# Kernel tuning notes

Measured on AMD Instinct MI355X. Metric: run time of the kernel, lower is better.

The kernel has to match this reference:

```python
import jax, jax.numpy as jnp
import numpy as np

HEADS = 8
DIM_HEAD = 40


def setup_inputs() -> dict:
    key = jax.random.key(0)
    ks = jax.random.split(key, 10)
    b, n, j, qd, cd = 8, 4096, 77, 320, 768
    inner = HEADS * DIM_HEAD  # 320
    x = jax.random.normal(ks[0], (b, n, qd), jnp.float32)
    embs = jax.random.normal(ks[1], (b, j, cd), jnp.float32)
    Wq = jax.random.normal(ks[2], (qd, inner), jnp.float32) * 0.02
    Wk = jax.random.normal(ks[3], (cd, inner), jnp.float32) * 0.02
    Wv = jax.random.normal(ks[4], (cd, inner), jnp.float32) * 0.02
    Wo = jax.random.normal(ks[5], (inner, qd), jnp.float32) * 0.02
    bo = jnp.zeros((qd,), jnp.float32)
    # per-query-token, per-key-token additive attention mask (float weights)
    cross_attn_mask = (jax.random.uniform(ks[6], (b, n, j)) < 0.5).astype(jnp.float32)
    strength = jnp.ones((1,), jnp.float32) * 0.8
    # captiontypes >= 0 marks valid key tokens; include some -1 (invalid)
    captiontypes = jax.random.randint(ks[7], (b, j), -1, 3).at[:, 0].set(0)
    global_prompt_mask = (jax.random.uniform(ks[8], (b, j)) > 0.05).at[:, 0].set(True)
    return {"x": x, "embs": embs, "Wq": Wq, "Wk": Wk, "Wv": Wv, "Wo": Wo,
            "bo": bo, "cross_attn_mask": cross_attn_mask, "strength": strength,
            "captiontypes": captiontypes, "global_prompt_mask": global_prompt_mask}


def _split_heads(t):
    # [b, n, h*d] -> [(b h), n, d], head index fastest (matches einops '(b h)')
    b, n, _ = t.shape
    return t.reshape(b, n, HEADS, DIM_HEAD).transpose(0, 2, 1, 3).reshape(b * HEADS, n, DIM_HEAD)


def reference(x, embs, Wq, Wk, Wv, Wo, bo, cross_attn_mask, strength,
              captiontypes, global_prompt_mask):
    b, n, _ = x.shape
    scale = DIM_HEAD ** -0.5
    q = _split_heads(x @ Wq).astype(jnp.float32)   # [(b h), n, d]
    k = _split_heads(embs @ Wk).astype(jnp.float32)  # [(b h), j, d]
    v = _split_heads(embs @ Wv)                      # [(b h), j, d]
    sim = jnp.einsum('bid,bjd->bij', q, k)           # [(b h), n, j] fp32

    NEG = -jnp.finfo(sim.dtype).max
    key_mask = captiontypes >= 0                     # [b, j]
    key_mask_bh = jnp.repeat(key_mask, HEADS, axis=0)[:, None, :]  # [(b h), 1, j]

    # masked std of sim over valid key positions (unbiased, ddof=1), no grad
    w = jnp.broadcast_to(key_mask_bh, sim.shape).astype(sim.dtype)
    cnt = jnp.sum(w)
    mean = jnp.sum(sim * w) / cnt
    var = jnp.sum(w * (sim - mean) ** 2) / (cnt - 1.0)
    simstd = jnp.sqrt(var)

    wf = cross_attn_mask * simstd * strength[0]      # [b, n, j]
    wf = jnp.where(global_prompt_mask[:, None, :], wf, NEG)
    wf = jnp.repeat(wf, HEADS, axis=0)               # [(b h), n, j]
    wf = jax.lax.stop_gradient(wf)

    sim = jnp.where(key_mask_bh, sim, NEG) + wf
    attn = jax.nn.softmax(sim * scale, axis=-1)
    out = jnp.einsum('bij,bjd->bid', attn, v)        # [(b h), n, d]
    out = out.reshape(b, HEADS, n, DIM_HEAD).transpose(0, 2, 1, 3).reshape(b, n, HEADS * DIM_HEAD)
    return out @ Wo + bo
```

## Files before the change

### kernel.cpp

```cpp
#include <hip/hip_runtime.h>
#include <hip/hip_bf16.h>
#include <math.h>

#define HEADS 8
#define DIMH 40
#define BB 8
#define NN 4096
#define JJ 77
#define CDIM 768
#define INNER 320
#define NEGF (-3.4028234663852886e38f)

using bf16 = __hip_bfloat16;
using f32x4 = __attribute__((ext_vector_type(4))) float;
using bf16x8 = __attribute__((ext_vector_type(8))) short;
using ushort8 = __attribute__((ext_vector_type(8))) unsigned short;
using ushort4v = __attribute__((ext_vector_type(4))) unsigned short;

__device__ __forceinline__ unsigned short f2u(float f){
    bf16 t = __float2bfloat16(f);
    return *reinterpret_cast<unsigned short*>(&t);
}
__device__ __forceinline__ float u2f(unsigned short u){
    unsigned int w = ((unsigned int)u) << 16;
    return __uint_as_float(w);
}

struct Stats { int validcnt; int gflag; float simstd; };

__global__ void prep_kernel(const int* ct, const int* gpm, Stats* st){
    __shared__ int sflag, scnt;
    if(threadIdx.x==0){ sflag=0; scnt=0; }
    __syncthreads();
    int lflag=0, lcnt=0;
    for(int i=threadIdx.x;i<154;i+=blockDim.x){
        int g = gpm[i];
        if(g!=0 && g!=1) lflag=1;
    }
    for(int i=threadIdx.x;i<BB*JJ;i+=blockDim.x){
        if(ct[i]>=0) lcnt++;
    }
    if(lflag) atomicOr(&sflag,1);
    atomicAdd(&scnt,lcnt);
    __syncthreads();
    if(threadIdx.x==0){ st->validcnt=scnt; st->gflag=sflag; }
}

__global__ __launch_bounds__(256) void prep_weights(const float* __restrict__ Wq,
                                                    const float* __restrict__ Wo,
                                                    const float* __restrict__ Wk,
                                                    const float* __restrict__ Wv,
                                                    unsigned short* __restrict__ WqT,
                                                    unsigned short* __restrict__ WoT,
                                                    unsigned short* __restrict__ WkvT){
    __shared__ float tile[32][33];
    int blk = blockIdx.x;
    int tx = threadIdx.x & 31, ty = threadIdx.x >> 5;
    if(blk < 200){
        const float* in = (blk<100)? Wq : Wo;
        unsigned short* out = (blk<100)? WqT : WoT;
        int base = (blk<100)? blk : blk-100;
        int bx = base%10, by = base/10;
        int c0 = bx*32, r0 = by*32;
        #pragma unroll
        for(int i=0;i<32;i+=8) tile[ty+i][tx] = in[(size_t)(r0+ty+i)*320 + c0+tx];
        __syncthreads();
        #pragma unroll
        for(int i=0;i<32;i+=8) out[(size_t)(c0+ty+i)*320 + r0+tx] = f2u(tile[tx][ty+i]);
    } else {
        int local = blk-200;
        int nt = local%20, kt = local/20;
        int n0 = nt*32, k0 = kt*32;
        const float* in = (n0<320)? Wk : Wv;
        int nc0 = (n0<320)? n0 : n0-320;
        #pragma unroll
        for(int i=0;i<32;i+=8) tile[ty+i][tx] = in[(size_t)(k0+ty+i)*320 + nc0+tx];
        __syncthreads();
        #pragma unroll
        for(int i=0;i<32;i+=8) WkvT[(size_t)(n0+ty+i)*768 + k0+tx] = f2u(tile[tx][ty+i]);
    }
}

__global__ __launch_bounds__(256) void proj_kv_mfma(const float* __restrict__ embs,
                                                    const unsigned short* __restrict__ WkvT,
                                                    unsigned short* __restrict__ kws,
                                                    unsigned short* __restrict__ vt){
    __shared__ unsigned short As[64][40];
    __shared__ unsigned short Bs[64][40];
    int t = threadIdx.x;
    int bm = blockIdx.x % 10;
    int bn = blockIdx.x / 10;
    int row0 = bm*64, col0 = bn*64;
    int wave=t>>6, lane=t&63, l15=lane&15, lk=lane>>4;

    f32x4 acc[4];
    #pragma unroll
    for(int nf=0;nf<4;nf++) acc[nf]=(f32x4){0.f,0.f,0.f,0.f};

    for(int k0=0;k0<768;k0+=32){
        #pragma unroll
        for(int p=0;p<2;p++){
            int li = (p*256+t)*4; int r = li>>5, kk = li&31;
            int gr = row0 + r;
            ushort4v u;
            if(gr < 616){
                float4 v = *(const float4*)&embs[(size_t)gr*768 + k0+kk];
                u.x=f2u(v.x); u.y=f2u(v.y); u.z=f2u(v.z); u.w=f2u(v.w);
            } else { u.x=0;u.y=0;u.z=0;u.w=0; }
            *(ushort4v*)&As[r][kk] = u;
        }
        {
            int nn = t>>2, kk = (t&3)*8;
            *(ushort8*)&Bs[nn][kk] = *(const ushort8*)&WkvT[(size_t)(col0+nn)*768 + k0+kk];
        }
        __syncthreads();
        bf16x8 aF = *(const bf16x8*)&As[wave*16+l15][lk*8];
        #pragma unroll
        for(int nf=0;nf<4;nf++){
            bf16x8 bF = *(const bf16x8*)&Bs[nf*16+l15][lk*8];
            acc[nf] = __builtin_amdgcn_mfma_f32_16x16x32_bf16(aF,bF,acc[nf],0,0,0);
        }
        __syncthreads();
    }
    #pragma unroll
    for(int nf=0;nf<4;nf++){
        int col = col0 + nf*16 + l15;
        #pragma unroll
        for(int r=0;r<4;r++){
            int m = row0 + wave*16 + lk*4 + r;
            if(m < 616){
                int b = m/77, j = m - 77*b;
                unsigned short val = f2u(acc[nf][r]);
                if(col < 320){
                    int h = col/40, d = col - 40*h;
                    kws[(((size_t)b*HEADS+h)*JJ + j)*DIMH + d] = val;
                } else {
                    int c2 = col-320; int h = c2/40, d = c2 - 40*h;
                    size_t vbase = (((size_t)b*HEADS+h)*DIMH + d)*80;
                    vt[vbase + j] = val;
                    if(j==76){ vt[vbase+77]=0; vt[vbase+78]=0; vt[vbase+79]=0; }
                }
            }
        }
    }
}

template<int A_MODE, int C_MODE>
__global__ __launch_bounds__(256) void gemm_mfma(const void* __restrict__ A,
                                                 const unsigned short* __restrict__ Bt,
                                                 const float* __restrict__ bias,
                                                 void* __restrict__ C){
    __shared__ unsigned short As[128][40];
    __shared__ unsigned short Bs[64][40];
    int t = threadIdx.x;
    int bm = blockIdx.x & 255;
    int bn = blockIdx.x >> 8;
    int row0 = bm*128, col0 = bn*64;
    int wave = t>>6, lane = t&63;
    int wm = wave>>1, wn = wave&1;
    int l15 = lane&15, lk = lane>>4;

    f32x4 acc[4][2];
    #pragma unroll
    for(int i=0;i<4;i++)
        #pragma unroll
        for(int j=0;j<2;j++) acc[i][j] = (f32x4){0.f,0.f,0.f,0.f};

    for(int k0=0;k0<320;k0+=32){
        if(A_MODE==2){
            const unsigned short* Ab = (const unsigned short*)A;
            #pragma unroll
            for(int p=0;p<2;p++){
                int li = (p*256+t)*8; int r = li>>5, kk = li&31;
                int m = row0+r; int k = k0+kk;
                int b = m>>12, n = m&4095;
                int h = k/40, d = k-40*h;
                *(ushort8*)&As[r][kk] = *(const ushort8*)&Ab[(((size_t)(b*8+h))*NN + n)*DIMH + d];
            }
        } else {
            const float* Af = (const float*)A;
            #pragma unroll
            for(int p=0;p<4;p++){
                int li = (p*256+t)*4; int r = li>>5, kk = li&31;
                float4 v = *(const float4*)&Af[(size_t)(row0+r)*320 + k0+kk];
                ushort4v u; u.x=f2u(v.x); u.y=f2u(v.y); u.z=f2u(v.z); u.w=f2u(v.w);
                *(ushort4v*)&As[r][kk] = u;
            }
        }
        {
            int nn = t>>2, kk = (t&3)*8;
            *(ushort8*)&Bs[nn][kk] = *(const ushort8*)&Bt[(size_t)(col0+nn)*320 + k0+kk];
        }
        __syncthreads();
        bf16x8 a[4], b[2];
        #pragma unroll
        for(int mf=0;mf<4;mf++) a[mf] = *(const bf16x8*)&As[wm*64+mf*16+l15][lk*8];
        #pragma unroll
        for(int nf=0;nf<2;nf++) b[nf] = *(const bf16x8*)&Bs[wn*32+nf*16+l15][lk*8];
        #pragma unroll
        for(int mf=0;mf<4;mf++)
            #pragma unroll
            for(int nf=0;nf<2;nf++)
                acc[mf][nf] = __builtin_amdgcn_mfma_f32_16x16x32_bf16(a[mf], b[nf], acc[mf][nf], 0,0,0);
        __syncthreads();
    }
    if(C_MODE==1){
        float* Cf = (float*)C;
        float bv[2];
        #pragma unroll
        for(int nf=0;nf<2;nf++) bv[nf] = bias[col0+wn*32+nf*16+l15];
        #pragma unroll
        for(int mf=0;mf<4;mf++)
            #pragma unroll
            for(int nf=0;nf<2;nf++){
                int col = col0+wn*32+nf*16+l15;
                #pragma unroll
                for(int r=0;r<4;r++){
                    int m = row0+wm*64+mf*16+lk*4+r;
                    Cf[(size_t)m*320+col] = acc[mf][nf][r] + bv[nf];
                }
            }
    } else {
        unsigned short* Cb = (unsigned short*)C;
        #pragma unroll
        for(int mf=0;mf<4;mf++)
            #pragma unroll
            for(int nf=0;nf<2;nf++){
                int col = col0+wn*32+nf*16+l15;
                int h = col/40, d = col-40*h;
                #pragma unroll
                for(int r=0;r<4;r++){
                    int m = row0+wm*64+mf*16+lk*4+r;
                    int b = m>>12, n = m&4095;
                    Cb[(((size_t)(b*8+h))*NN + n)*DIMH + d] = f2u(acc[mf][nf][r]);
                }
            }
    }
}

__global__ __launch_bounds__(256) void stats_mfma(const unsigned short* __restrict__ qh,
                                                  const unsigned short* __restrict__ kws,
                                                  const int* __restrict__ ct,
                                                  float2* __restrict__ partials){
    int bh = blockIdx.x;
    int b = bh>>3;
    int t = threadIdx.x;
    int wave=t>>6, lane=t&63, l15=lane&15, lk=lane>>4;
    int wq0 = wave*16;
    bf16x8 zb = {0,0,0,0,0,0,0,0};

    int n0 = blockIdx.y*64;
    size_t qrow = ((size_t)bh*NN + n0 + wq0 + l15)*DIMH;
    bf16x8 aF0 = *(const bf16x8*)&qh[qrow + lk*8];
    bf16x8 aF1 = (lk==0) ? *(const bf16x8*)&qh[qrow + 32] : zb;

    bool kv[5];
    bf16x8 bK[2][5];
    #pragma unroll
    for(int jt=0;jt<5;jt++){
        int j = jt*16+l15;
        kv[jt] = (j<JJ) && (ct[b*JJ+j]>=0);
        #pragma unroll
        for(int ks=0;ks<2;ks++){
            if(j<JJ && !(ks==1 && lk>=1))
                bK[ks][jt] = *(const bf16x8*)&kws[((size_t)bh*JJ + j)*DIMH + ks*32 + lk*8];
            else bK[ks][jt] = zb;
        }
    }
    f32x4 sacc[5];
    #pragma unroll
    for(int jt=0;jt<5;jt++) sacc[jt]=(f32x4){0.f,0.f,0.f,0.f};
    #pragma unroll
    for(int jt=0;jt<5;jt++){
        sacc[jt] = __builtin_amdgcn_mfma_f32_16x16x32_bf16(aF0,bK[0][jt],sacc[jt],0,0,0);
        sacc[jt] = __builtin_amdgcn_mfma_f32_16x16x32_bf16(aF1,bK[1][jt],sacc[jt],0,0,0);
    }
    float s1=0.f, s2=0.f;
    #pragma unroll
    for(int jt=0;jt<5;jt++){
        if(kv[jt]){
            #pragma unroll
            for(int r=0;r<4;r++){ float v=sacc[jt][r]; s1+=v; s2+=v*v; }
        }
    }
    #pragma unroll
    for(int off=32;off>0;off>>=1){ s1 += __shfl_down(s1,off); s2 += __shfl_down(s2,off); }
    __shared__ float sa[4], sb[4];
    if(lane==0){ sa[wave]=s1; sb[wave]=s2; }
    __syncthreads();
    if(t==0){
        partials[blockIdx.y*64 + blockIdx.x] =
            make_float2(sa[0]+sa[1]+sa[2]+sa[3], sb[0]+sb[1]+sb[2]+sb[3]);
    }
}

__global__ __launch_bounds__(256) void finalize_kernel(const float2* __restrict__ partials,
                                                       const int* __restrict__ ct,
                                                       const int* __restrict__ gpm,
                                                       const float* __restrict__ strength,
                                                       Stats* st,
                                                       float* __restrict__ kmT,
                                                       float* __restrict__ adT,
                                                       float* __restrict__ gmT){
    int t = threadIdx.x;
    double s1=0.0, s2=0.0;
    for(int i=t;i<4096;i+=256){
        float2 p = partials[i];
        s1 += (double)p.x; s2 += (double)p.y;
    }
    #pragma unroll
    for(int off=32;off>0;off>>=1){ s1 += __shfl_down(s1,off); s2 += __shfl_down(s2,off); }
    __shared__ double da[4], db[4];
    __shared__ float s_simstd;
    int lane=t&63, w=t>>6;
    if(lane==0){ da[w]=s1; db[w]=s2; }
    __syncthreads();
    if(t==0){
        double S1 = da[0]+da[1]+da[2]+da[3];
        double S2 = db[0]+db[1]+db[2]+db[3];
        double cnt = (double)st->validcnt * HEADS * NN;
        double var = (S2 - S1*S1/cnt)/(cnt-1.0);
        float sd = (float)sqrt(var);
        st->simstd = sd;
        s_simstd = sd;
    }
    __syncthreads();
    float c = s_simstd * strength[0];
    int gflag = st->gflag;
    for(int i=t;i<BB*80;i+=256){
        int b = i/80, j = i-80*b;
        int kvv=0, gv=0;
        if(j<JJ){
            kvv = ct[b*JJ+j]>=0;
            gv = gflag ? (((const unsigned char*)gpm)[b*JJ+j]!=0) : (gpm[b*JJ+j]!=0);
        }
        kmT[i] = (j<JJ && kvv)?1.f:0.f;
        adT[i] = ((j<JJ && kvv)?0.f:NEGF) + ((j<JJ && gv)?0.f:NEGF);
        gmT[i] = (j<JJ && gv)? c : 0.f;
    }
}

__global__ __launch_bounds__(256) void attn_mfma(unsigned short* qh,
                                                 const unsigned short* __restrict__ kws,
                                                 const unsigned short* __restrict__ vt,
                                                 const float* __restrict__ cam,
                                                 const float* __restrict__ kmT,
                                                 const float* __restrict__ adT,
                                                 const float* __restrict__ gmT){
    int bh = blockIdx.x;
    int b = bh>>3;
    __shared__ unsigned short P[64][104];
    int t = threadIdx.x;
    int wave=t>>6, lane=t&63, l15=lane&15, lk=lane>>4;
    int wq0 = wave*16;
    bf16x8 zb = {0,0,0,0,0,0,0,0};
    ushort8 z8 = {0,0,0,0,0,0,0,0};

    int n0 = blockIdx.y*64;
    size_t qrow = ((size_t)bh*NN + n0 + wq0 + l15)*DIMH;
    bf16x8 aF0 = *(const bf16x8*)&qh[qrow + lk*8];
    bf16x8 aF1 = (lk==0) ? *(const bf16x8*)&qh[qrow + 32] : zb;

    float cv[5][4];
    #pragma unroll
    for(int jt=0;jt<5;jt++){
        int j = jt*16+l15; int jc = (j<JJ)? j : 76;
        #pragma unroll
        for(int r=0;r<4;r++){
            int row = n0 + wq0 + 4*lk + r;
            cv[jt][r] = cam[((size_t)b*NN+row)*JJ + jc];
        }
    }
    float km[5], gm[5], ad[5];
    #pragma unroll
    for(int jt=0;jt<5;jt++){
        int j = jt*16+l15;
        km[jt] = kmT[b*80+j]; ad[jt] = adT[b*80+j]; gm[jt] = gmT[b*80+j];
    }
    bf16x8 bK[2][5];
    #pragma unroll
    for(int ks=0;ks<2;ks++)
        #pragma unroll
        for(int jt=0;jt<5;jt++){
            int j = jt*16+l15;
            if(j<JJ && !(ks==1 && lk>=1))
                bK[ks][jt] = *(const bf16x8*)&kws[((size_t)bh*JJ + j)*DIMH + ks*32 + lk*8];
            else bK[ks][jt] = zb;
        }
    bf16x8 bV[3][3];
    #pragma unroll
    for(int ks=0;ks<3;ks++)
        #pragma unroll
        for(int nt=0;nt<3;nt++){
            int d = nt*16+l15;
            if(d<DIMH && !(ks==2 && lk>=2))
                bV[ks][nt] = *(const bf16x8*)&vt[((size_t)bh*DIMH + d)*80 + ks*32 + lk*8];
            else bV[ks][nt] = zb;
        }
    if(t<64){ *(ushort8*)&P[t][80]=z8; *(ushort8*)&P[t][88]=z8; *(ushort8*)&P[t][96]=z8; }

    const float scale = 0.15811388300841897f;
    f32x4 sacc[5];
    #pragma unroll
    for(int jt=0;jt<5;jt++) sacc[jt]=(f32x4){0.f,0.f,0.f,0.f};
    #pragma unroll
    for(int jt=0;jt<5;jt++){
        sacc[jt] = __builtin_amdgcn_mfma_f32_16x16x32_bf16(aF0,bK[0][jt],sacc[jt],0,0,0);
        sacc[jt] = __builtin_amdgcn_mfma_f32_16x16x32_bf16(aF1,bK[1][jt],sacc[jt],0,0,0);
    }
    float lo[5][4];
    #pragma unroll
    for(int jt=0;jt<5;jt++){
        #pragma unroll
        for(int r=0;r<4;r++)
            lo[jt][r] = (sacc[jt][r]*km[jt] + cv[jt][r]*gm[jt] + ad[jt])*scale;
    }
    float dinv[4];
    #pragma unroll
    for(int r=0;r<4;r++){
        float m = lo[0][r];
        #pragma unroll
        for(int jt=1;jt<5;jt++) m = fmaxf(m, lo[jt][r]);
        #pragma unroll
        for(int msk=1;msk<16;msk<<=1) m = fmaxf(m, __shfl_xor(m,msk));
        float s=0.f;
        #pragma unroll
        for(int jt=0;jt<5;jt++){ float e=__expf(lo[jt][r]-m); lo[jt][r]=e; s+=e; }
        #pragma unroll
        for(int msk=1;msk<16;msk<<=1) s += __shfl_xor(s,msk);
        dinv[r]=1.f/s;
    }
    #pragma unroll
    for(int jt=0;jt<5;jt++){
        int j = jt*16+l15;
        #pragma unroll
        for(int r=0;r<4;r++) P[wq0+4*lk+r][j] = f2u(lo[jt][r]*dinv[r]);
    }
    __syncthreads();
    f32x4 oacc[3];
    #pragma unroll
    for(int nt=0;nt<3;nt++) oacc[nt]=(f32x4){0.f,0.f,0.f,0.f};
    #pragma unroll
    for(int ks=0;ks<3;ks++){
        bf16x8 aP = *(const bf16x8*)&P[wq0+l15][ks*32+lk*8];
        #pragma unroll
        for(int nt=0;nt<3;nt++)
            oacc[nt] = __builtin_amdgcn_mfma_f32_16x16x32_bf16(aP,bV[ks][nt],oacc[nt],0,0,0);
    }
    #pragma unroll
    for(int nt=0;nt<3;nt++){
        int d = nt*16+l15;
        #pragma unroll
        for(int r=0;r<4;r++){
            unsigned short ush = f2u(oacc[nt][r]);
            int other = __shfl_xor((int)ush, 1);
            if((l15&1)==0 && d<DIMH){
                unsigned int word = (unsigned int)ush | (((unsigned int)(unsigned short)other)<<16);
                int row = n0 + wq0 + 4*lk + r;
                *(unsigned int*)&qh[((size_t)bh*NN + row)*DIMH + d] = word;
            }
        }
    }
}

extern "C" void kernel_launch(void* const* d_in, const int* in_sizes, int n_in,
                              void* d_out, int out_size, void* d_ws, size_t ws_size,
                              hipStream_t stream) {
    const float* x        = (const float*)d_in[0];
    const float* embs     = (const float*)d_in[1];
    const float* Wq       = (const float*)d_in[2];
    const float* Wk       = (const float*)d_in[3];
    const float* Wv       = (const float*)d_in[4];
    const float* Wo       = (const float*)d_in[5];
    const float* bo       = (const float*)d_in[6];
    const float* cam      = (const float*)d_in[7];
    const float* strength = (const float*)d_in[8];
    const int*  ct       = (const int*)d_in[9];
    const int*  gpm      = (const int*)d_in[10];

    char* ws = (char*)d_ws;
    unsigned short* qh   = (unsigned short*)ws;
    unsigned short* kws  = (unsigned short*)(ws + 20971520);
    unsigned short* vt   = (unsigned short*)(ws + 21365760);
    unsigned short* WqT  = (unsigned short*)(ws + 21775360);
    unsigned short* WoT  = (unsigned short*)(ws + 21980160);
    unsigned short* WkvT = (unsigned short*)(ws + 22184960);
    Stats* st  = (Stats*)(ws + 23168000);
    float2* partials = (float2*)(ws + 23169024);
    float* kmT = (float*)(ws + 23201792);
    float* adT = (float*)(ws + 23204352);
    float* gmT = (float*)(ws + 23206912);

    prep_kernel<<<1,256,0,stream>>>(ct,gpm,st);
    prep_weights<<<680,256,0,stream>>>(Wq,Wo,Wk,Wv,WqT,WoT,WkvT);
    proj_kv_mfma<<<100,256,0,stream>>>(embs,WkvT,kws,vt);
    gemm_mfma<0,2><<<1280,256,0,stream>>>(x,WqT,nullptr,qh);
    stats_mfma<<<dim3(64,64),256,0,stream>>>(qh,kws,ct,partials);
    finalize_kernel<<<1,256,0,stream>>>(partials,ct,gpm,strength,st,kmT,adT,gmT);
    attn_mfma<<<dim3(64,64),256,0,stream>>>(qh,kws,vt,cam,kmT,adT,gmT);
    gemm_mfma<2,1><<<1280,256,0,stream>>>(qh,WoT,bo,d_out);
}
```

Baseline: 130.2 us.

## Enlarge GEMM tile to 256x64 and fold prep kernel into finalize

The projection GEMMs now use 256-row tiles, with each wave computing a 64x64 output block, which halves the block count and reuses each B fragment across more rows. The separate prep_kernel launch is removed; its valid-count and flag computation moves into finalize_kernel. This saves a launch and reduces redundant B loads, at the cost of more accumulator registers and fewer blocks to spread across CUs.

```diff
diff --git a/kernel.cpp b/kernel.cpp
--- a/kernel.cpp
+++ b/kernel.cpp
@@ -27,24 +27,6 @@
 }
 
 struct Stats { int validcnt; int gflag; float simstd; };
-
-__global__ void prep_kernel(const int* ct, const int* gpm, Stats* st){
-    __shared__ int sflag, scnt;
-    if(threadIdx.x==0){ sflag=0; scnt=0; }
-    __syncthreads();
-    int lflag=0, lcnt=0;
-    for(int i=threadIdx.x;i<154;i+=blockDim.x){
-        int g = gpm[i];
-        if(g!=0 && g!=1) lflag=1;
-    }
-    for(int i=threadIdx.x;i<BB*JJ;i+=blockDim.x){
-        if(ct[i]>=0) lcnt++;
-    }
-    if(lflag) atomicOr(&sflag,1);
-    atomicAdd(&scnt,lcnt);
-    __syncthreads();
-    if(threadIdx.x==0){ st->validcnt=scnt; st->gflag=sflag; }
-}
 
 __global__ __launch_bounds__(256) void prep_weights(const float* __restrict__ Wq,
                                                     const float* __restrict__ Wo,
@@ -150,27 +132,26 @@
                                                  const unsigned short* __restrict__ Bt,
                                                  const float* __restrict__ bias,
                                                  void* __restrict__ C){
-    __shared__ unsigned short As[128][40];
+    __shared__ unsigned short As[256][40];
     __shared__ unsigned short Bs[64][40];
     int t = threadIdx.x;
-    int bm = blockIdx.x & 255;
-    int bn = blockIdx.x >> 8;
-    int row0 = bm*128, col0 = bn*64;
+    int bm = blockIdx.x & 127;
+    int bn = blockIdx.x >> 7;
+    int row0 = bm*256, col0 = bn*64;
     int wave = t>>6, lane = t&63;
-    int wm = wave>>1, wn = wave&1;
     int l15 = lane&15, lk = lane>>4;
 
-    f32x4 acc[4][2];
+    f32x4 acc[4][4];
     #pragma unroll
     for(int i=0;i<4;i++)
         #pragma unroll
-        for(int j=0;j<2;j++) acc[i][j] = (f32x4){0.f,0.f,0.f,0.f};
+        for(int j=0;j<4;j++) acc[i][j] = (f32x4){0.f,0.f,0.f,0.f};
 
     for(int k0=0;k0<320;k0+=32){
         if(A_MODE==2){
             const unsigned short* Ab = (const unsigned short*)A;
             #pragma unroll
-            for(int p=0;p<2;p++){
+            for(int p=0;p<4;p++){
                 int li = (p*256+t)*8; int r = li>>5, kk = li&31;
                 int m = row0+r; int k = k0+kk;
                 int b = m>>12, n = m&4095;
@@ -180,7 +161,7 @@
         } else {
             const float* Af = (const float*)A;
             #pragma unroll
-            for(int p=0;p<4;p++){
+            for(int p=0;p<8;p++){
                 int li = (p*256+t)*4; int r = li>>5, kk = li&31;
                 float4 v = *(const float4*)&Af[(size_t)(row0+r)*320 + k0+kk];
                 ushort4v u; u.x=f2u(v.x); u.y=f2u(v.y); u.z=f2u(v.z); u.w=f2u(v.w);
@@ -192,31 +173,31 @@
             *(ushort8*)&Bs[nn][kk] = *(const ushort8*)&Bt[(size_t)(col0+nn)*320 + k0+kk];
         }
         __syncthreads();
-        bf16x8 a[4], b[2];
-        #pragma unroll
-        for(int mf=0;mf<4;mf++) a[mf] = *(const bf16x8*)&As[wm*64+mf*16+l15][lk*8];
-        #pragma unroll
-        for(int nf=0;nf<2;nf++) b[nf] = *(const bf16x8*)&Bs[wn*32+nf*16+l15][lk*8];
+        bf16x8 a[4], b[4];
+        #pragma unroll
+        for(int mf=0;mf<4;mf++) a[mf] = *(const bf16x8*)&As[wave*64+mf*16+l15][lk*8];
+        #pragma unroll
+        for(int nf=0;nf<4;nf++) b[nf] = *(const bf16x8*)&Bs[nf*16+l15][lk*8];
         #pragma unroll
         for(int mf=0;mf<4;mf++)
             #pragma unroll
-            for(int nf=0;nf<2;nf++)
+            for(int nf=0;nf<4;nf++)
                 acc[mf][nf] = __builtin_amdgcn_mfma_f32_16x16x32_bf16(a[mf], b[nf], acc[mf][nf], 0,0,0);
         __syncthreads();
     }
     if(C_MODE==1){
         float* Cf = (float*)C;
-        float bv[2];
-        #pragma unroll
-        for(int nf=0;nf<2;nf++) bv[nf] = bias[col0+wn*32+nf*16+l15];
+        float bv[4];
+        #pragma unroll
+        for(int nf=0;nf<4;nf++) bv[nf] = bias[col0+nf*16+l15];
         #pragma unroll
         for(int mf=0;mf<4;mf++)
             #pragma unroll
-            for(int nf=0;nf<2;nf++){
-                int col = col0+wn*32+nf*16+l15;
+            for(int nf=0;nf<4;nf++){
+                int col = col0+nf*16+l15;
                 #pragma unroll
                 for(int r=0;r<4;r++){
-                    int m = row0+wm*64+mf*16+lk*4+r;
+                    int m = row0+wave*64+mf*16+lk*4+r;
                     Cf[(size_t)m*320+col] = acc[mf][nf][r] + bv[nf];
                 }
             }
@@ -225,12 +206,12 @@
         #pragma unroll
         for(int mf=0;mf<4;mf++)
             #pragma unroll
-            for(int nf=0;nf<2;nf++){
-                int col = col0+wn*32+nf*16+l15;
+            for(int nf=0;nf<4;nf++){
+                int col = col0+nf*16+l15;
                 int h = col/40, d = col-40*h;
                 #pragma unroll
                 for(int r=0;r<4;r++){
-                    int m = row0+wm*64+mf*16+lk*4+r;
+                    int m = row0+wave*64+mf*16+lk*4+r;
                     int b = m>>12, n = m&4095;
                     Cb[(((size_t)(b*8+h))*NN + n)*DIMH + d] = f2u(acc[mf][nf][r]);
                 }
@@ -303,6 +284,14 @@
                                                        float* __restrict__ adT,
                                                        float* __restrict__ gmT){
     int t = threadIdx.x;
+    __shared__ int sflag, scnt;
+    if(t==0){ sflag=0; scnt=0; }
+    __syncthreads();
+    int lflag=0, lcnt=0;
+    for(int i=t;i<154;i+=256){ int g = gpm[i]; if(g!=0 && g!=1) lflag=1; }
+    for(int i=t;i<BB*JJ;i+=256){ if(ct[i]>=0) lcnt++; }
+    if(lflag) atomicOr(&sflag,1);
+    atomicAdd(&scnt,lcnt);
     double s1=0.0, s2=0.0;
     for(int i=t;i<4096;i+=256){
         float2 p = partials[i];
@@ -318,15 +307,15 @@
     if(t==0){
         double S1 = da[0]+da[1]+da[2]+da[3];
         double S2 = db[0]+db[1]+db[2]+db[3];
-        double cnt = (double)st->validcnt * HEADS * NN;
+        double cnt = (double)scnt * HEADS * NN;
         double var = (S2 - S1*S1/cnt)/(cnt-1.0);
         float sd = (float)sqrt(var);
-        st->simstd = sd;
+        st->validcnt = scnt; st->gflag = sflag; st->simstd = sd;
         s_simstd = sd;
     }
     __syncthreads();
     float c = s_simstd * strength[0];
-    int gflag = st->gflag;
+    int gflag = sflag;
     for(int i=t;i<BB*80;i+=256){
         int b = i/80, j = i-80*b;
         int kvv=0, gv=0;
@@ -491,12 +480,11 @@
     float* adT = (float*)(ws + 23204352);
     float* gmT = (float*)(ws + 23206912);
 
-    prep_kernel<<<1,256,0,stream>>>(ct,gpm,st);
     prep_weights<<<680,256,0,stream>>>(Wq,Wo,Wk,Wv,WqT,WoT,WkvT);
     proj_kv_mfma<<<100,256,0,stream>>>(embs,WkvT,kws,vt);
-    gemm_mfma<0,2><<<1280,256,0,stream>>>(x,WqT,nullptr,qh);
+    gemm_mfma<0,2><<<640,256,0,stream>>>(x,WqT,nullptr,qh);
     stats_mfma<<<dim3(64,64),256,0,stream>>>(qh,kws,ct,partials);
     finalize_kernel<<<1,256,0,stream>>>(partials,ct,gpm,strength,st,kmT,adT,gmT);
     attn_mfma<<<dim3(64,64),256,0,stream>>>(qh,kws,vt,cam,kmT,adT,gmT);
-    gemm_mfma<2,1><<<1280,256,0,stream>>>(qh,WoT,bo,d_out);
-}
+    gemm_mfma<2,1><<<640,256,0,stream>>>(qh,WoT,bo,d_out);
+}
```

Result: no change. 128.5 us (-1.3%).
